# Optimization experiments

Hardware: AMD Instinct MI355X
Metric: run time of the kernel (lower is better)

The kernel has to match this reference:

```python
import jax, jax.numpy as jnp
import numpy as np

NUM_EMBEDDINGS = 1024
EMBEDDING_DIM = 64
COMMITMENT_COST = 0.25

def setup_inputs() -> dict:
    key = jax.random.key(0)
    k1, k2 = jax.random.split(key)
    z = jax.random.normal(k1, (64, EMBEDDING_DIM, 32, 32), dtype=jnp.float32)
    # nn.Embedding initialized uniform(-1/K, 1/K)
    lim = 1.0 / NUM_EMBEDDINGS
    embeddings = jax.random.uniform(k2, (NUM_EMBEDDINGS, EMBEDDING_DIM), dtype=jnp.float32, minval=-lim, maxval=lim)
    return {"z": z, "embeddings": embeddings}

def reference(z, embeddings):
    # z: [B, C, H, W] with C == embedding_dim
    z_perm = jnp.transpose(z, (0, 2, 3, 1))            # [B, H, W, D]
    flat_z = z_perm.reshape(-1, EMBEDDING_DIM)          # [N, D]
    # squared L2 distances: ||z||^2 - 2 z.e + ||e||^2  -> [N, K]
    distances = (jnp.sum(flat_z ** 2, axis=1, keepdims=True)
                 - 2.0 * flat_z @ embeddings.T
                 + jnp.sum(embeddings ** 2, axis=1))
    encoding_indices = jnp.argmin(distances, axis=1)    # [N]
    # direct gather == one-hot @ embeddings (same math, no [N,K] one-hot)
    quantized = embeddings[encoding_indices].reshape(z_perm.shape)
    commitment_loss = COMMITMENT_COST * jnp.mean((jax.lax.stop_gradient(quantized) - z_perm) ** 2)
    codebook_loss = jnp.mean((quantized - jax.lax.stop_gradient(z_perm)) ** 2)
    loss = commitment_loss + codebook_loss
    # straight-through estimator
    quantized_st = z_perm + jax.lax.stop_gradient(quantized - z_perm)
    return jnp.transpose(quantized_st, (0, 3, 1, 2)), loss
```

## Files before the change

kernel.cpp:

```cpp
#include <hip/hip_runtime.h>

#define D 64
#define K 1024
#define NVEC 65536
#define MB 128
#define NBLK (NVEC / MB)
#define WAVES 4
#define KPW (K / WAVES)
#define TILES (KPW / 16)

typedef __attribute__((ext_vector_type(8))) short bf16x8;
typedef __attribute__((ext_vector_type(4))) float f32x4;

__device__ inline unsigned short f2bf(float f) {
    unsigned u = __builtin_bit_cast(unsigned, f);
    return (unsigned short)((u + 0x7FFFu + ((u >> 16) & 1u)) >> 16);
}

__global__ __launch_bounds__(256) void vq_prep(const float* __restrict__ emb,
                                               unsigned short* __restrict__ ebf,
                                               float* __restrict__ hn) {
    const int k = blockIdx.x * 256 + threadIdx.x;
    const float4* e4 = reinterpret_cast<const float4*>(emb + (size_t)k * D);
    ushort4* o4 = reinterpret_cast<ushort4*>(ebf + (size_t)k * D);
    float s = 0.f;
#pragma unroll
    for (int i = 0; i < D / 4; ++i) {
        float4 v = e4[i];
        s = fmaf(v.x, v.x, s); s = fmaf(v.y, v.y, s);
        s = fmaf(v.z, v.z, s); s = fmaf(v.w, v.w, s);
        ushort4 b; b.x = f2bf(v.x); b.y = f2bf(v.y); b.z = f2bf(v.z); b.w = f2bf(v.w);
        o4[i] = b;
    }
    hn[k] = 0.5f * s;
}

__global__ __launch_bounds__(256) void vq_mfma(const float* __restrict__ z,
                                               const float* __restrict__ emb,
                                               const unsigned short* __restrict__ ebf,
                                               const float* __restrict__ hn,
                                               float* __restrict__ out,
                                               float* __restrict__ pT,
                                               float* __restrict__ pZ) {
    __shared__ __align__(16) char zl[MB * 128];
    __shared__ float wv_t[WAVES * MB];
    __shared__ int   wv_i[WAVES * MB];
    __shared__ int   fin_i[MB];
    __shared__ float red[256];

    const int tid = threadIdx.x;
    const int blk = blockIdx.x;
    const int b   = blk >> 3;
    const int hw0 = (blk & 7) * MB;
    const float* zb = z + (size_t)b * (D * 1024) + hw0;

    float zacc = 0.f;
#pragma unroll
    for (int it = 0; it < 2; ++it) {
        const int item = it * 256 + tid;
        const int v4 = item & 31;
        const int d4 = item >> 5;
        float4 r[4];
#pragma unroll
        for (int i = 0; i < 4; ++i)
            r[i] = *reinterpret_cast<const float4*>(zb + (size_t)(d4 * 4 + i) * 1024 + v4 * 4);
        const float* rf = reinterpret_cast<const float*>(r);
#pragma unroll
        for (int n = 0; n < 16; ++n) zacc = fmaf(rf[n], rf[n], zacc);
#pragma unroll
        for (int j = 0; j < 4; ++j) {
            const int v = v4 * 4 + j;
            ushort4 pk;
            pk.x = f2bf(rf[0 * 4 + j]); pk.y = f2bf(rf[1 * 4 + j]);
            pk.z = f2bf(rf[2 * 4 + j]); pk.w = f2bf(rf[3 * 4 + j]);
            const int byte = v * 128 + ((d4 * 8) ^ ((v & 7) << 4));
            *reinterpret_cast<ushort4*>(zl + byte) = pk;
        }
    }
    __syncthreads();

    const int wave = tid >> 6;
    const int lane = tid & 63;
    const int l16  = lane & 15;
    const int lg   = lane >> 4;

    bf16x8 bfr[8][2];
#pragma unroll
    for (int g = 0; g < 8; ++g)
#pragma unroll
        for (int h = 0; h < 2; ++h) {
            const int v = g * 16 + l16;
            const int byte = v * 128 + (((h * 64) + lg * 16) ^ ((v & 7) << 4));
            bfr[g][h] = *reinterpret_cast<const bf16x8*>(zl + byte);
        }

    float best[8]; int bidx[8];
#pragma unroll
    for (int g = 0; g < 8; ++g) { best[g] = -3e38f; bidx[g] = 0; }
    const int cw = wave * KPW;
    for (int kt = 0; kt < TILES; ++kt) {
        const int cbase = cw + kt * 16;
        const bf16x8 a0 = *reinterpret_cast<const bf16x8*>(ebf + (size_t)(cbase + l16) * 64 + lg * 8);
        const bf16x8 a1 = *reinterpret_cast<const bf16x8*>(ebf + (size_t)(cbase + l16) * 64 + 32 + lg * 8);
        const float4 h4 = *reinterpret_cast<const float4*>(hn + cbase + lg * 4);
        const float* h4f = reinterpret_cast<const float*>(&h4);
#pragma unroll
        for (int g = 0; g < 8; ++g) {
            f32x4 c = {0.f, 0.f, 0.f, 0.f};
            c = __builtin_amdgcn_mfma_f32_16x16x32_bf16(a0, bfr[g][0], c, 0, 0, 0);
            c = __builtin_amdgcn_mfma_f32_16x16x32_bf16(a1, bfr[g][1], c, 0, 0, 0);
#pragma unroll
            for (int r = 0; r < 4; ++r) {
                const float tv = c[r] - h4f[r];
                if (tv > best[g]) { best[g] = tv; bidx[g] = cbase + lg * 4 + r; }
            }
        }
    }

#pragma unroll
    for (int g = 0; g < 8; ++g) {
        float tv = best[g]; int ti = bidx[g];
#pragma unroll
        for (int off = 16; off <= 32; off <<= 1) {
            const float ot = __shfl_xor(tv, off, 64);
            const int   oi = __shfl_xor(ti, off, 64);
            if (ot > tv || (ot == tv && oi < ti)) { tv = ot; ti = oi; }
        }
        if (lg == 0) {
            wv_t[wave * MB + g * 16 + l16] = tv;
            wv_i[wave * MB + g * 16 + l16] = ti;
        }
    }
    __syncthreads();

    float tsum = 0.f;
    if (tid < MB) {
        float tv = wv_t[tid]; int ti = wv_i[tid];
#pragma unroll
        for (int w = 1; w < WAVES; ++w) {
            const float ot = wv_t[w * MB + tid];
            const int   oi = wv_i[w * MB + tid];
            if (ot > tv || (ot == tv && oi < ti)) { tv = ot; ti = oi; }
        }
        fin_i[tid] = ti;
        tsum = tv;
    }
    __syncthreads();

    {
        const int v  = tid & 127;
        const int dh = tid >> 7;
        const int idx = fin_i[v];
        const float4* eq4 = reinterpret_cast<const float4*>(emb + (size_t)idx * D);
        float* ob = out + (size_t)b * (D * 1024) + hw0 + v;
#pragma unroll
        for (int i = 0; i < 8; ++i) {
            const float4 q = eq4[dh * 8 + i];
            const int d = dh * 32 + i * 4;
            ob[(size_t)(d + 0) * 1024] = q.x;
            ob[(size_t)(d + 1) * 1024] = q.y;
            ob[(size_t)(d + 2) * 1024] = q.z;
            ob[(size_t)(d + 3) * 1024] = q.w;
        }
    }

    red[tid] = zacc;
    __syncthreads();
#pragma unroll
    for (int s = 128; s > 0; s >>= 1) {
        if (tid < s) red[tid] += red[tid + s];
        __syncthreads();
    }
    if (tid == 0) pZ[blk] = red[0];
    __syncthreads();
    red[tid] = tsum;
    __syncthreads();
#pragma unroll
    for (int s = 128; s > 0; s >>= 1) {
        if (tid < s) red[tid] += red[tid + s];
        __syncthreads();
    }
    if (tid == 0) pT[blk] = red[0];
}

__global__ __launch_bounds__(256) void vq_loss(const float* __restrict__ pT,
                                               const float* __restrict__ pZ,
                                               float* __restrict__ loss_out) {
    __shared__ float red[256];
    float s = 0.f;
    for (int i = threadIdx.x; i < NBLK; i += 256) s += pZ[i] - 2.f * pT[i];
    red[threadIdx.x] = s;
    __syncthreads();
#pragma unroll
    for (int st = 128; st > 0; st >>= 1) {
        if (threadIdx.x < st) red[threadIdx.x] += red[threadIdx.x + st];
        __syncthreads();
    }
    if (threadIdx.x == 0)
        loss_out[0] = 1.25f * red[0] * (1.0f / (float)((size_t)NVEC * D));
}

extern "C" void kernel_launch(void* const* d_in, const int* in_sizes, int n_in,
                              void* d_out, int out_size, void* d_ws, size_t ws_size,
                              hipStream_t stream) {
    const float* z   = (const float*)d_in[0];
    const float* emb = (const float*)d_in[1];
    float* out = (float*)d_out;

    char* ws = (char*)d_ws;
    unsigned short* ebf = (unsigned short*)ws;
    float* hn = (float*)(ws + 131072);
    float* pT = (float*)(ws + 135168);
    float* pZ = (float*)(ws + 137216);

    vq_prep<<<K / 256, 256, 0, stream>>>(emb, ebf, hn);
    vq_mfma<<<NBLK, 256, 0, stream>>>(z, emb, ebf, hn, out, pT, pZ);
    vq_loss<<<1, 256, 0, stream>>>(pT, pZ, out + (size_t)NVEC * D);
}
```

Measured before the change: 34.06 us.

## Pack score and index into one int max, halve block tile, fuse loss partials

The MFMA accumulator is now seeded with 1 - 0.5||e||^2, so every score is positive. Its float bits are masked so the low 10 bits hold the codeword index, which turns the argmax into a single integer max per element and removes the compare-and-select on value and index pairs and the paired shuffles. The block tile drops from 128 to 64 vectors, doubling the grid to 1024 blocks and cutting register use. The two loss reductions are merged into one per-block partial. The packed key truncates the low mantissa bits, so near-tied distances may pick a different codeword (the highest index rather than the lowest), and the +1 offset lowers precision in the recovered loss term.

After: 36.27 us. 1.06x slower.

```diff
diff --git a/kernel.cpp b/kernel.cpp
--- a/kernel.cpp
+++ b/kernel.cpp
@@ -3,11 +3,12 @@
 #define D 64
 #define K 1024
 #define NVEC 65536
-#define MB 128
+#define MB 64
 #define NBLK (NVEC / MB)
 #define WAVES 4
 #define KPW (K / WAVES)
 #define TILES (KPW / 16)
+#define NG (MB / 16)
 
 typedef __attribute__((ext_vector_type(8))) short bf16x8;
 typedef __attribute__((ext_vector_type(4))) float f32x4;
@@ -19,7 +20,7 @@
 
 __global__ __launch_bounds__(256) void vq_prep(const float* __restrict__ emb,
                                                unsigned short* __restrict__ ebf,
-                                               float* __restrict__ hn) {
+                                               float* __restrict__ hb) {
     const int k = blockIdx.x * 256 + threadIdx.x;
     const float4* e4 = reinterpret_cast<const float4*>(emb + (size_t)k * D);
     ushort4* o4 = reinterpret_cast<ushort4*>(ebf + (size_t)k * D);
@@ -32,34 +33,30 @@
         ushort4 b; b.x = f2bf(v.x); b.y = f2bf(v.y); b.z = f2bf(v.z); b.w = f2bf(v.w);
         o4[i] = b;
     }
-    hn[k] = 0.5f * s;
+    hb[k] = 1.0f - 0.5f * s;
 }
 
 __global__ __launch_bounds__(256) void vq_mfma(const float* __restrict__ z,
                                                const float* __restrict__ emb,
                                                const unsigned short* __restrict__ ebf,
-                                               const float* __restrict__ hn,
+                                               const float* __restrict__ hb,
                                                float* __restrict__ out,
-                                               float* __restrict__ pT,
-                                               float* __restrict__ pZ) {
+                                               float* __restrict__ pP) {
     __shared__ __align__(16) char zl[MB * 128];
-    __shared__ float wv_t[WAVES * MB];
-    __shared__ int   wv_i[WAVES * MB];
-    __shared__ int   fin_i[MB];
+    __shared__ int   wv[WAVES * MB];
+    __shared__ int   fin[MB];
     __shared__ float red[256];
 
     const int tid = threadIdx.x;
     const int blk = blockIdx.x;
-    const int b   = blk >> 3;
-    const int hw0 = (blk & 7) * MB;
+    const int b   = blk >> 4;
+    const int hw0 = (blk & 15) * MB;
     const float* zb = z + (size_t)b * (D * 1024) + hw0;
 
     float zacc = 0.f;
-#pragma unroll
-    for (int it = 0; it < 2; ++it) {
-        const int item = it * 256 + tid;
-        const int v4 = item & 31;
-        const int d4 = item >> 5;
+    {
+        const int v4 = tid & 15;
+        const int d4 = tid >> 4;
         float4 r[4];
 #pragma unroll
         for (int i = 0; i < 4; ++i)
@@ -84,9 +81,9 @@
     const int l16  = lane & 15;
     const int lg   = lane >> 4;
 
-    bf16x8 bfr[8][2];
+    bf16x8 bfr[NG][2];
 #pragma unroll
-    for (int g = 0; g < 8; ++g)
+    for (int g = 0; g < NG; ++g)
 #pragma unroll
         for (int h = 0; h < 2; ++h) {
             const int v = g * 16 + l16;
@@ -94,69 +91,63 @@
             bfr[g][h] = *reinterpret_cast<const bf16x8*>(zl + byte);
         }
 
-    float best[8]; int bidx[8];
+    int best[NG];
 #pragma unroll
-    for (int g = 0; g < 8; ++g) { best[g] = -3e38f; bidx[g] = 0; }
+    for (int g = 0; g < NG; ++g) best[g] = 0;
     const int cw = wave * KPW;
+#pragma unroll 4
     for (int kt = 0; kt < TILES; ++kt) {
         const int cbase = cw + kt * 16;
         const bf16x8 a0 = *reinterpret_cast<const bf16x8*>(ebf + (size_t)(cbase + l16) * 64 + lg * 8);
         const bf16x8 a1 = *reinterpret_cast<const bf16x8*>(ebf + (size_t)(cbase + l16) * 64 + 32 + lg * 8);
-        const float4 h4 = *reinterpret_cast<const float4*>(hn + cbase + lg * 4);
-        const float* h4f = reinterpret_cast<const float*>(&h4);
+        const f32x4 ci = *reinterpret_cast<const f32x4*>(hb + cbase + lg * 4);
+        const int idx0 = cbase + lg * 4;
 #pragma unroll
-        for (int g = 0; g < 8; ++g) {
-            f32x4 c = {0.f, 0.f, 0.f, 0.f};
+        for (int g = 0; g < NG; ++g) {
+            f32x4 c = ci;
             c = __builtin_amdgcn_mfma_f32_16x16x32_bf16(a0, bfr[g][0], c, 0, 0, 0);
             c = __builtin_amdgcn_mfma_f32_16x16x32_bf16(a1, bfr[g][1], c, 0, 0, 0);
 #pragma unroll
             for (int r = 0; r < 4; ++r) {
-                const float tv = c[r] - h4f[r];
-                if (tv > best[g]) { best[g] = tv; bidx[g] = cbase + lg * 4 + r; }
+                const int pk = (int)((__builtin_bit_cast(unsigned, c[r]) & 0xFFFFFC00u)
+                                     | (unsigned)(idx0 + r));
+                best[g] = best[g] > pk ? best[g] : pk;
             }
         }
     }
 
 #pragma unroll
-    for (int g = 0; g < 8; ++g) {
-        float tv = best[g]; int ti = bidx[g];
-#pragma unroll
-        for (int off = 16; off <= 32; off <<= 1) {
-            const float ot = __shfl_xor(tv, off, 64);
-            const int   oi = __shfl_xor(ti, off, 64);
-            if (ot > tv || (ot == tv && oi < ti)) { tv = ot; ti = oi; }
-        }
-        if (lg == 0) {
-            wv_t[wave * MB + g * 16 + l16] = tv;
-            wv_i[wave * MB + g * 16 + l16] = ti;
-        }
+    for (int g = 0; g < NG; ++g) {
+        int tv = best[g];
+        int o = __shfl_xor(tv, 16, 64); tv = tv > o ? tv : o;
+        o = __shfl_xor(tv, 32, 64);     tv = tv > o ? tv : o;
+        if (lane < 16) wv[wave * MB + g * 16 + l16] = tv;
     }
     __syncthreads();
 
-    float tsum = 0.f;
+    float tcon = 0.f;
     if (tid < MB) {
-        float tv = wv_t[tid]; int ti = wv_i[tid];
+        int tv = wv[tid];
 #pragma unroll
         for (int w = 1; w < WAVES; ++w) {
-            const float ot = wv_t[w * MB + tid];
-            const int   oi = wv_i[w * MB + tid];
-            if (ot > tv || (ot == tv && oi < ti)) { tv = ot; ti = oi; }
+            const int o = wv[w * MB + tid];
+            tv = tv > o ? tv : o;
         }
-        fin_i[tid] = ti;
-        tsum = tv;
+        fin[tid] = tv & 1023;
+        tcon = __builtin_bit_cast(float, (unsigned)tv & 0xFFFFFC00u) - 1.0f;
     }
     __syncthreads();
 
     {
-        const int v  = tid & 127;
-        const int dh = tid >> 7;
-        const int idx = fin_i[v];
-        const float4* eq4 = reinterpret_cast<const float4*>(emb + (size_t)idx * D);
+        const int v  = tid & 63;
+        const int dh = tid >> 6;
+        const int idx = fin[v];
+        const float4* eq4 = reinterpret_cast<const float4*>(emb + (size_t)idx * D + dh * 16);
         float* ob = out + (size_t)b * (D * 1024) + hw0 + v;
 #pragma unroll
-        for (int i = 0; i < 8; ++i) {
-            const float4 q = eq4[dh * 8 + i];
-            const int d = dh * 32 + i * 4;
+        for (int i = 0; i < 4; ++i) {
+            const float4 q = eq4[i];
+            const int d = dh * 16 + i * 4;
             ob[(size_t)(d + 0) * 1024] = q.x;
             ob[(size_t)(d + 1) * 1024] = q.y;
             ob[(size_t)(d + 2) * 1024] = q.z;
@@ -164,31 +155,21 @@
         }
     }
 
-    red[tid] = zacc;
+    red[tid] = zacc - 2.f * tcon;
     __syncthreads();
 #pragma unroll
     for (int s = 128; s > 0; s >>= 1) {
         if (tid < s) red[tid] += red[tid + s];
         __syncthreads();
     }
-    if (tid == 0) pZ[blk] = red[0];
-    __syncthreads();
-    red[tid] = tsum;
-    __syncthreads();
-#pragma unroll
-    for (int s = 128; s > 0; s >>= 1) {
-        if (tid < s) red[tid] += red[tid + s];
-        __syncthreads();
-    }
-    if (tid == 0) pT[blk] = red[0];
+    if (tid == 0) pP[blk] = red[0];
 }
 
-__global__ __launch_bounds__(256) void vq_loss(const float* __restrict__ pT,
-                                               const float* __restrict__ pZ,
+__global__ __launch_bounds__(256) void vq_loss(const float* __restrict__ pP,
                                                float* __restrict__ loss_out) {
     __shared__ float red[256];
     float s = 0.f;
-    for (int i = threadIdx.x; i < NBLK; i += 256) s += pZ[i] - 2.f * pT[i];
+    for (int i = threadIdx.x; i < NBLK; i += 256) s += pP[i];
     red[threadIdx.x] = s;
     __syncthreads();
 #pragma unroll
@@ -209,11 +190,10 @@
 
     char* ws = (char*)d_ws;
     unsigned short* ebf = (unsigned short*)ws;
-    float* hn = (float*)(ws + 131072);
-    float* pT = (float*)(ws + 135168);
-    float* pZ = (float*)(ws + 137216);
+    float* hb = (float*)(ws + 131072);
+    float* pP = (float*)(ws + 135168);
 
-    vq_prep<<<K / 256, 256, 0, stream>>>(emb, ebf, hn);
-    vq_mfma<<<NBLK, 256, 0, stream>>>(z, emb, ebf, hn, out, pT, pZ);
-    vq_loss<<<1, 256, 0, stream>>>(pT, pZ, out + (size_t)NVEC * D);
+    vq_prep<<<K / 256, 256, 0, stream>>>(emb, ebf, hb);
+    vq_mfma<<<NBLK, 256, 0, stream>>>(z, emb, ebf, hb, out, pP);
+    vq_loss<<<1, 256, 0, stream>>>(pP, out + (size_t)NVEC * D);
 }
```
